# Kernel optimization log

Measured on AMD Instinct MI355X. Metric: run time of the kernel, lower is better.

Reference implementation:

```python
import jax, jax.numpy as jnp
import numpy as np

N_NODES = 100000
IN_DIM = 64
OUT_DIM = 64
N_EDGES = 1600000


def _undirected_self_loops(edge_index, num_nodes):
    """Symmetrize, add self loops, coalesce (dedup+sort) like the torch module.
    edge_index is an integer constant, so we preprocess with numpy (no grads flow here).
    Returns (src, dst, w) where w are symmetric GCN normalization weights.
    """
    ei = np.asarray(edge_index, dtype=np.int64)
    loops = np.arange(num_nodes, dtype=np.int64)
    full_src = np.concatenate([ei[0], ei[1], loops])
    full_dst = np.concatenate([ei[1], ei[0], loops])
    keys = np.unique(full_src * num_nodes + full_dst)  # coalesce, sorted
    src = keys // num_nodes
    dst = keys % num_nodes
    deg = np.bincount(dst, minlength=num_nodes).clip(min=1)
    inv_sqrt = deg.astype(np.float32) ** -0.5
    w = inv_sqrt[src] * inv_sqrt[dst]
    return src, dst, w


def setup_inputs() -> dict:
    key = jax.random.key(0)
    kx, kw, kb, ke = jax.random.split(key, 4)
    x = jax.random.normal(kx, (N_NODES, IN_DIM), dtype=jnp.float32)
    # nn.Linear params: W (out, in), b (out,)
    W = jax.random.normal(kw, (OUT_DIM, IN_DIM), dtype=jnp.float32) / np.sqrt(IN_DIM)
    b = jax.random.normal(kb, (OUT_DIM,), dtype=jnp.float32) * 0.01
    edge_index = jax.random.randint(ke, (2, N_EDGES), 0, N_NODES, dtype=jnp.int64)
    return {"x": x, "edge_index": edge_index, "W": W, "b": b}


def reference(x, edge_index, W, b) -> jnp.ndarray:
    n = x.shape[0]
    src_np, dst_np, w_np = _undirected_self_loops(edge_index, n)
    src = jnp.asarray(src_np)
    dst = jnp.asarray(dst_np)
    w = jnp.asarray(w_np).astype(x.dtype)  # (E',)
    h = x @ W.T + b                         # (N, out_dim)
    msg = h[src] * w[:, None]               # gather + per-edge scale, (E', out_dim)
    out = jnp.zeros_like(h).at[dst].add(msg)  # scatter-add aggregation
    return out
```

## Files before the change

kernel.cpp:

```cpp
#include <hip/hip_runtime.h>
#include <hip/hip_bf16.h>
#include <stdint.h>

#define NN 100000
#define EE 1600000
#define CAP 128
#define NB 782
#define CAPB 5120
#define HTS 8192
#define EMPTY 0xFFFFFFFFu
#define BIN_CHUNK 2048
#define GL 782
#define GB 782

__device__ __forceinline__ unsigned int mix32(unsigned int x){
  x ^= x >> 16; x *= 0x7feb352du;
  x ^= x >> 15; x *= 0x846ca68bu;
  x ^= x >> 16;
  return x;
}

extern "C" __global__ __launch_bounds__(256)
void k_prep(const float* __restrict__ x, const float* __restrict__ W,
            const float* __restrict__ bias, __hip_bfloat16* __restrict__ hb,
            const int* __restrict__ ei, int* __restrict__ bcnt,
            unsigned int* __restrict__ bbuf){
  __shared__ __align__(16) char sm[51200];
  const int tid = threadIdx.x;

  if (!(blockIdx.x & 1)){
    const int lb = blockIdx.x >> 1;
    float (*wt)[64] = reinterpret_cast<float(*)[64]>(sm);
    float (*xs)[68] = reinterpret_cast<float(*)[68]>(sm + 16384);
    const int lane = tid & 63;
    const int w    = tid >> 6;
    #pragma unroll
    for (int r = 0; r < 16; ++r){
      int i = r*4 + w;
      wt[i][lane] = W[lane*64 + i];
    }
    const int nbase = lb * 128;
    #pragma unroll
    for (int r = 0; r < 8; ++r){
      int idx = r*256 + tid;
      int nl  = idx >> 4;
      int c4  = idx & 15;
      int n   = nbase + nl;
      float4 v = make_float4(0.f,0.f,0.f,0.f);
      if (n < NN) v = reinterpret_cast<const float4*>(x)[(size_t)n*16 + c4];
      *reinterpret_cast<float4*>(&xs[nl][c4*4]) = v;
    }
    __syncthreads();

    const int og  = tid & 7;
    const int nl0 = (tid >> 3) * 4;
    float acc[4][8];
    #pragma unroll
    for (int t=0;t<4;++t){
      #pragma unroll
      for (int j=0;j<8;++j) acc[t][j]=0.f;
    }
    #pragma unroll 4
    for (int i=0;i<64;++i){
      float4 wa = *reinterpret_cast<const float4*>(&wt[i][og*8]);
      float4 wb = *reinterpret_cast<const float4*>(&wt[i][og*8+4]);
      #pragma unroll
      for (int t=0;t<4;++t){
        float xv = xs[nl0+t][i];
        acc[t][0] += xv*wa.x; acc[t][1] += xv*wa.y;
        acc[t][2] += xv*wa.z; acc[t][3] += xv*wa.w;
        acc[t][4] += xv*wb.x; acc[t][5] += xv*wb.y;
        acc[t][6] += xv*wb.z; acc[t][7] += xv*wb.w;
      }
    }
    float4 b0 = reinterpret_cast<const float4*>(bias)[og*2];
    float4 b1 = reinterpret_cast<const float4*>(bias)[og*2+1];
    float bb[8] = {b0.x,b0.y,b0.z,b0.w,b1.x,b1.y,b1.z,b1.w};
    #pragma unroll
    for (int t=0;t<4;++t){
      int n = nbase + nl0 + t;
      if (n < NN){
        union { uint4 u4; __hip_bfloat16 v[8]; } pk;
        #pragma unroll
        for (int j=0;j<8;++j) pk.v[j] = __float2bfloat16(acc[t][j] + bb[j]);
        reinterpret_cast<uint4*>(&hb[(size_t)n*64])[og] = pk.u4;
      }
    }
  } else {
    const int bb_id = blockIdx.x >> 1;
    int* hist  = reinterpret_cast<int*>(sm);
    int* bbase = hist + NB;
    int* bcur  = bbase + NB;
    for (int i = tid; i < NB; i += 256) hist[i] = 0;
    __syncthreads();
    const int e0 = bb_id * BIN_CHUNK;
    #pragma unroll 1
    for (int r = 0; r < BIN_CHUNK; r += 256){
      int i = e0 + r + tid;
      if (i < EE){
        int a = ei[i], c = ei[EE + i];
        atomicAdd(&hist[c >> 7], 1);
        atomicAdd(&hist[a >> 7], 1);
      }
    }
    __syncthreads();
    for (int bk = tid; bk < NB; bk += 256){
      int hh = hist[bk];
      bbase[bk] = hh ? atomicAdd(&bcnt[bk], hh) : 0;
      bcur[bk]  = 0;
    }
    __syncthreads();
    #pragma unroll 1
    for (int r = 0; r < BIN_CHUNK; r += 256){
      int i = e0 + r + tid;
      if (i < EE){
        int a = ei[i], c = ei[EE + i];
        int b1 = c >> 7, b2 = a >> 7;
        int p1 = bbase[b1] + atomicAdd(&bcur[b1], 1);
        int p2 = bbase[b2] + atomicAdd(&bcur[b2], 1);
        if (p1 < CAPB) bbuf[(size_t)b1*CAPB + p1] = ((unsigned)a << 7) | (unsigned)(c & 127);
        if (p2 < CAPB) bbuf[(size_t)b2*CAPB + p2] = ((unsigned)c << 7) | (unsigned)(a & 127);
      }
    }
  }
}

extern "C" __global__ __launch_bounds__(256)
void k_dedup(const int* __restrict__ bcnt, const unsigned int* __restrict__ bbuf,
             unsigned int* __restrict__ srclist, int* __restrict__ cnt,
             float* __restrict__ inv){
  __shared__ unsigned int HT[HTS];
  __shared__ int dcur[128];
  const int tid = threadIdx.x;
  const int b   = blockIdx.x;
  const int d0  = b << 7;
  for (int i = tid; i < HTS; i += 256) HT[i] = EMPTY;
  if (tid < 128) dcur[tid] = 0;
  __syncthreads();

  int n = bcnt[b]; if (n > CAPB) n = CAPB;
  const unsigned int* buf = bbuf + (size_t)b * CAPB;
  for (int k = tid; k < n; k += 256){
    unsigned int pk  = buf[k];
    unsigned int idx = mix32(pk) & (HTS-1);
    for (;;){
      unsigned int prev = atomicCAS(&HT[idx], EMPTY, pk);
      if (prev == EMPTY || prev == pk) break;
      idx = (idx + 1) & (HTS-1);
    }
  }
  if (tid < 128 && d0 + tid < NN){
    unsigned int pk  = ((unsigned)(d0 + tid) << 7) | (unsigned)tid;
    unsigned int idx = mix32(pk) & (HTS-1);
    for (;;){
      unsigned int prev = atomicCAS(&HT[idx], EMPTY, pk);
      if (prev == EMPTY || prev == pk) break;
      idx = (idx + 1) & (HTS-1);
    }
  }
  __syncthreads();

  for (int i = tid; i < HTS; i += 256){
    unsigned int v = HT[i];
    if (v != EMPTY){
      int dl  = v & 127;
      int pos = atomicAdd(&dcur[dl], 1);
      if (pos < CAP) srclist[(size_t)(d0 + dl) * CAP + pos] = v >> 7;
    }
  }
  __syncthreads();
  if (tid < 128 && d0 + tid < NN){
    int c = dcur[tid];
    cnt[d0 + tid] = c;
    inv[d0 + tid] = rsqrtf((float)c);
  }
}

extern "C" __global__ __launch_bounds__(256)
void k_agg(const __hip_bfloat16* __restrict__ hb, const float* __restrict__ inv,
           const int* __restrict__ cnt, const unsigned int* __restrict__ srclist,
           float* __restrict__ out){
  __shared__ uint2 sv[4][CAP];
  const int wv   = threadIdx.x >> 6;
  const int lane = threadIdx.x & 63;
  const int half = lane >> 5;
  const int pl   = lane & 31;
  const int d    = blockIdx.x*4 + wv;
  if (d >= NN) return;
  const unsigned int* reg = srclist + (size_t)d * CAP;
  int c = cnt[d]; if (c > CAP) c = CAP;
  const int c16 = (c + 15) & ~15;

  if (lane < c){
    unsigned s = reg[lane];
    sv[wv][lane] = make_uint2(s, __float_as_uint(inv[s]));
  }
  if (64 + lane < c){
    unsigned s = reg[64 + lane];
    sv[wv][64 + lane] = make_uint2(s, __float_as_uint(inv[s]));
  }
  { int p = c + lane; if (p < c16) sv[wv][p] = make_uint2(0u, 0u); }

  const char* hbase = (const char*)hb;
  const int   boff  = pl << 2;
  float ax[8], ay[8];
  #pragma unroll
  for (int u=0;u<8;++u){ ax[u]=0.f; ay[u]=0.f; }
  #pragma unroll 1
  for (int j = 0; j < c16; j += 16){
    #pragma unroll
    for (int u = 0; u < 8; ++u){
      uint2 e = sv[wv][j + 2*u + half];
      float w = __uint_as_float(e.y);
      unsigned hv = *reinterpret_cast<const unsigned*>(hbase + ((size_t)e.x << 7) + boff);
      ax[u] += w * __uint_as_float(hv << 16);
      ay[u] += w * __uint_as_float(hv & 0xFFFF0000u);
    }
  }
  float rx = ((ax[0]+ax[1])+(ax[2]+ax[3])) + ((ax[4]+ax[5])+(ax[6]+ax[7]));
  float ry = ((ay[0]+ay[1])+(ay[2]+ay[3])) + ((ay[4]+ay[5])+(ay[6]+ay[7]));
  rx += __shfl_xor(rx, 32);
  ry += __shfl_xor(ry, 32);
  if (half == 0){
    float iv = inv[d];
    float2 o = make_float2(rx * iv, ry * iv);
    *reinterpret_cast<float2*>(&out[(size_t)d*64 + (pl << 1)]) = o;
  }
}

extern "C" void kernel_launch(void* const* d_in, const int* in_sizes, int n_in,
                              void* d_out, int out_size, void* d_ws, size_t ws_size,
                              hipStream_t stream){
  (void)in_sizes; (void)n_in; (void)out_size; (void)ws_size;
  const float* x  = (const float*)d_in[0];
  const int*   ei = (const int*)  d_in[1];
  const float* W  = (const float*)d_in[2];
  const float* b  = (const float*)d_in[3];
  float* out = (float*)d_out;

  char* ws = (char*)d_ws;
  __hip_bfloat16* hb      = (__hip_bfloat16*)ws;
  float*          inv     = (float*)(ws + 12800000);
  int*            cnt     = (int*)  (ws + 13200000);
  unsigned int*   srclist = (unsigned int*)(ws + 13600000);
  int*            bcnt    = (int*)  (ws + 64800000);
  unsigned int*   bbuf    = (unsigned int*)(ws + 64804096);

  hipMemsetAsync(bcnt, 0, NB * 4, stream);

  k_prep  <<<GL + GB, 256, 0, stream>>>(x, W, b, hb, ei, bcnt, bbuf);
  k_dedup <<<NB, 256, 0, stream>>>(bcnt, bbuf, srclist, cnt, inv);
  k_agg   <<<(NN + 3)/4, 256, 0, stream>>>(hb, inv, cnt, srclist, out);
}
```

Baseline: 156.4 us.

## Rebalance prep kernel: smaller linear tiles, larger register-cached binning chunks

The fused prep kernel now uses 64-node linear tiles (1563 blocks) with x staged transposed in bf16 shared memory, and 4096-edge binning chunks (391 blocks) that keep edge endpoints in registers instead of reloading them. Blocks are interleaved 4:1 by a new index mapping, and hash-table init in dedup uses vectorized stores. The aim is to cut shared memory per block for higher occupancy, avoid the second global read of edge_index, and balance work across the fused launch. Rounding x to bf16 before the matmul adds precision loss, and 32 extra live registers in the binning path may reduce occupancy.

```diff
diff --git a/kernel.cpp b/kernel.cpp
--- a/kernel.cpp
+++ b/kernel.cpp
@@ -9,9 +9,8 @@
 #define CAPB 5120
 #define HTS 8192
 #define EMPTY 0xFFFFFFFFu
-#define BIN_CHUNK 2048
-#define GL 782
-#define GB 782
+#define GLIN 1563
+#define GBIN 391
 
 __device__ __forceinline__ unsigned int mix32(unsigned int x){
   x ^= x >> 16; x *= 0x7feb352du;
@@ -25,38 +24,45 @@
             const float* __restrict__ bias, __hip_bfloat16* __restrict__ hb,
             const int* __restrict__ ei, int* __restrict__ bcnt,
             unsigned int* __restrict__ bbuf){
-  __shared__ __align__(16) char sm[51200];
+  __shared__ __align__(16) char sm[25088];
   const int tid = threadIdx.x;
-
-  if (!(blockIdx.x & 1)){
-    const int lb = blockIdx.x >> 1;
-    float (*wt)[64] = reinterpret_cast<float(*)[64]>(sm);
-    float (*xs)[68] = reinterpret_cast<float(*)[68]>(sm + 16384);
+  const int bid = blockIdx.x;
+  bool isbin; int sub;
+  if (bid < 1950){ isbin = ((bid % 5) == 4); sub = isbin ? (bid/5) : (bid - bid/5); }
+  else if (bid < 1953){ isbin = false; sub = bid - 390; }
+  else { isbin = true; sub = 390; }
+
+  if (!isbin){
+    float (*wt)[64]           = reinterpret_cast<float(*)[64]>(sm);
+    __hip_bfloat16 (*xs)[68]  = reinterpret_cast<__hip_bfloat16(*)[68]>(sm + 16384);
     const int lane = tid & 63;
-    const int w    = tid >> 6;
+    const int wv   = tid >> 6;
     #pragma unroll
     for (int r = 0; r < 16; ++r){
-      int i = r*4 + w;
+      int i = r*4 + wv;
       wt[i][lane] = W[lane*64 + i];
     }
-    const int nbase = lb * 128;
-    #pragma unroll
-    for (int r = 0; r < 8; ++r){
+    const int nbase = sub * 64;
+    #pragma unroll
+    for (int r = 0; r < 4; ++r){
       int idx = r*256 + tid;
       int nl  = idx >> 4;
       int c4  = idx & 15;
       int n   = nbase + nl;
       float4 v = make_float4(0.f,0.f,0.f,0.f);
       if (n < NN) v = reinterpret_cast<const float4*>(x)[(size_t)n*16 + c4];
-      *reinterpret_cast<float4*>(&xs[nl][c4*4]) = v;
+      xs[c4*4+0][nl] = __float2bfloat16(v.x);
+      xs[c4*4+1][nl] = __float2bfloat16(v.y);
+      xs[c4*4+2][nl] = __float2bfloat16(v.z);
+      xs[c4*4+3][nl] = __float2bfloat16(v.w);
     }
     __syncthreads();
 
     const int og  = tid & 7;
-    const int nl0 = (tid >> 3) * 4;
-    float acc[4][8];
-    #pragma unroll
-    for (int t=0;t<4;++t){
+    const int nl0 = (tid >> 3) * 2;
+    float acc[2][8];
+    #pragma unroll
+    for (int t=0;t<2;++t){
       #pragma unroll
       for (int j=0;j<8;++j) acc[t][j]=0.f;
     }
@@ -64,20 +70,19 @@
     for (int i=0;i<64;++i){
       float4 wa = *reinterpret_cast<const float4*>(&wt[i][og*8]);
       float4 wb = *reinterpret_cast<const float4*>(&wt[i][og*8+4]);
-      #pragma unroll
-      for (int t=0;t<4;++t){
-        float xv = xs[nl0+t][i];
-        acc[t][0] += xv*wa.x; acc[t][1] += xv*wa.y;
-        acc[t][2] += xv*wa.z; acc[t][3] += xv*wa.w;
-        acc[t][4] += xv*wb.x; acc[t][5] += xv*wb.y;
-        acc[t][6] += xv*wb.z; acc[t][7] += xv*wb.w;
-      }
+      unsigned xv = *reinterpret_cast<const unsigned*>(&xs[i][nl0]);
+      float x0 = __uint_as_float(xv << 16);
+      float x1 = __uint_as_float(xv & 0xFFFF0000u);
+      acc[0][0] += x0*wa.x; acc[0][1] += x0*wa.y; acc[0][2] += x0*wa.z; acc[0][3] += x0*wa.w;
+      acc[0][4] += x0*wb.x; acc[0][5] += x0*wb.y; acc[0][6] += x0*wb.z; acc[0][7] += x0*wb.w;
+      acc[1][0] += x1*wa.x; acc[1][1] += x1*wa.y; acc[1][2] += x1*wa.z; acc[1][3] += x1*wa.w;
+      acc[1][4] += x1*wb.x; acc[1][5] += x1*wb.y; acc[1][6] += x1*wb.z; acc[1][7] += x1*wb.w;
     }
     float4 b0 = reinterpret_cast<const float4*>(bias)[og*2];
     float4 b1 = reinterpret_cast<const float4*>(bias)[og*2+1];
     float bb[8] = {b0.x,b0.y,b0.z,b0.w,b1.x,b1.y,b1.z,b1.w};
     #pragma unroll
-    for (int t=0;t<4;++t){
+    for (int t=0;t<2;++t){
       int n = nbase + nl0 + t;
       if (n < NN){
         union { uint4 u4; __hip_bfloat16 v[8]; } pk;
@@ -87,21 +92,21 @@
       }
     }
   } else {
-    const int bb_id = blockIdx.x >> 1;
     int* hist  = reinterpret_cast<int*>(sm);
     int* bbase = hist + NB;
     int* bcur  = bbase + NB;
     for (int i = tid; i < NB; i += 256) hist[i] = 0;
     __syncthreads();
-    const int e0 = bb_id * BIN_CHUNK;
-    #pragma unroll 1
-    for (int r = 0; r < BIN_CHUNK; r += 256){
-      int i = e0 + r + tid;
+    const int e0 = sub * 4096;
+    int ra[16], rc[16];
+    #pragma unroll
+    for (int r = 0; r < 16; ++r){
+      int i = e0 + r*256 + tid;
       if (i < EE){
-        int a = ei[i], c = ei[EE + i];
-        atomicAdd(&hist[c >> 7], 1);
-        atomicAdd(&hist[a >> 7], 1);
-      }
+        ra[r] = ei[i]; rc[r] = ei[EE + i];
+        atomicAdd(&hist[rc[r] >> 7], 1);
+        atomicAdd(&hist[ra[r] >> 7], 1);
+      } else ra[r] = -1;
     }
     __syncthreads();
     for (int bk = tid; bk < NB; bk += 256){
@@ -110,11 +115,10 @@
       bcur[bk]  = 0;
     }
     __syncthreads();
-    #pragma unroll 1
-    for (int r = 0; r < BIN_CHUNK; r += 256){
-      int i = e0 + r + tid;
-      if (i < EE){
-        int a = ei[i], c = ei[EE + i];
+    #pragma unroll
+    for (int r = 0; r < 16; ++r){
+      if (ra[r] >= 0){
+        int a = ra[r], c = rc[r];
         int b1 = c >> 7, b2 = a >> 7;
         int p1 = bbase[b1] + atomicAdd(&bcur[b1], 1);
         int p2 = bbase[b2] + atomicAdd(&bcur[b2], 1);
@@ -134,7 +138,9 @@
   const int tid = threadIdx.x;
   const int b   = blockIdx.x;
   const int d0  = b << 7;
-  for (int i = tid; i < HTS; i += 256) HT[i] = EMPTY;
+  uint4* HT4 = reinterpret_cast<uint4*>(HT);
+  #pragma unroll
+  for (int r = 0; r < 8; ++r) HT4[r*256 + tid] = make_uint4(EMPTY,EMPTY,EMPTY,EMPTY);
   if (tid < 128) dcur[tid] = 0;
   __syncthreads();
 
@@ -248,7 +254,7 @@
 
   hipMemsetAsync(bcnt, 0, NB * 4, stream);
 
-  k_prep  <<<GL + GB, 256, 0, stream>>>(x, W, b, hb, ei, bcnt, bbuf);
+  k_prep  <<<GLIN + GBIN, 256, 0, stream>>>(x, W, b, hb, ei, bcnt, bbuf);
   k_dedup <<<NB, 256, 0, stream>>>(bcnt, bbuf, srclist, cnt, inv);
   k_agg   <<<(NN + 3)/4, 256, 0, stream>>>(hb, inv, cnt, srclist, out);
 }
```

Result: faster. 142.2 us (-9.1%).
